# Optimization experiments

Measured on AMD Instinct MI355X. Metric: run time of the kernel, lower is better.

## Reference

```python
import jax, jax.numpy as jnp
import numpy as np

N_BUSES = 2000
W1, W2, W3, LMBDA = 1.0, 1.0, 1.0, 0.1


def setup_inputs() -> dict:
    key = jax.random.key(0)
    k0, k1, k2, k3, k4 = jax.random.split(key, 5)
    B, E = 32, 6000
    x = jax.random.normal(k0, (B * N_BUSES, 6), jnp.float32)
    edge_attr = jax.random.normal(k1, (B * E, 2), jnp.float32)
    edge_index = jax.random.randint(k2, (2, B * E), 0, N_BUSES)
    outputs = jax.random.normal(k3, (B * N_BUSES, 2), jnp.float32)
    labels = jax.random.normal(k4, (B * N_BUSES, 2), jnp.float32)
    return {"x": x, "edge_attr": edge_attr, "edge_index": edge_index,
            "outputs": outputs, "labels": labels}


def _physics_terms(x, edge_attr, edge_index, outputs):
    B = x.shape[0] // N_BUSES
    # Vpred: complex voltage prediction, (B, N, 1)
    Vpred = (outputs[:, 0] + 1j * outputs[:, 1]).astype(jnp.complex64)
    Vpred = Vpred.reshape(B, N_BUSES, 1)
    nf = x.reshape(B, N_BUSES, 6)
    ea = edge_attr.reshape(B, -1, 2)
    E = ea.shape[1]
    ei = edge_index.reshape(2, B, E) % N_BUSES  # (2, B, E)
    S = (nf[:, :, 0] + 1j * nf[:, :, 1]).astype(jnp.complex64)  # (B, N)
    Vm = nf[:, :, 2]
    bus_type = nf[:, :, 3:6]
    adm = (ea[:, :, 0] + 1j * ea[:, :, 1]).astype(jnp.complex64)  # (B, E)
    # scatter edge admittances into dense Y (B, N, N)
    b_idx = jnp.arange(B)[:, None]
    Y = jnp.zeros((B, N_BUSES, N_BUSES), jnp.complex64)
    Y = Y.at[b_idx, ei[0], ei[1]].set(adm)
    # Spred = V * conj(Y @ V)
    YV = jnp.matmul(Y, Vpred)                      # (B, N, 1)
    Spred = (Vpred * jnp.conj(YV))[:, :, 0]        # (B, N)
    S_mean = jnp.mean(S, axis=1, keepdims=True)
    S_inverse = jnp.where(S != 0, 1.0 / S, 1.0 / S_mean)
    S_inverse_norm = jnp.abs(S_inverse)
    result1 = ((Spred - S) ** 2) * bus_type[:, :, 0]                    # complex
    result2 = ((Spred.real - S.real) ** 2) * bus_type[:, :, 1]          # real
    Vm_mean = jnp.mean(Vm, axis=1, keepdims=True)
    Vm_inverse = jnp.where(Vm != 0, 1.0 / Vm, 1.0 / Vm_mean)
    D1 = S_inverse_norm * (result1 + result2)                           # complex
    Vmag = jnp.abs(Vpred[:, :, 0])
    D2 = jnp.abs(Vmag * (bus_type[:, :, 1] + bus_type[:, :, 2]) - Vm) * Vm_inverse
    D3 = jnp.abs(Vpred[:, :, 0].imag * bus_type[:, :, 2]) * Vm_inverse
    return jnp.mean(D1), jnp.mean(D2), jnp.mean(D3)


def reference(x, edge_attr, edge_index, outputs, labels):
    d1, d2, d3 = _physics_terms(x, edge_attr, edge_index, outputs)
    physics_loss = W1 * d1 + W2 * d2 + W3 * d3  # complex (D1 is complex, as in torch)
    mse = jnp.mean((outputs - labels) ** 2)
    loss = mse + LMBDA * physics_loss
    return loss, physics_loss, d1, d2, d3
```

## Files before the change

### kernel.cpp

```cpp
#include <hip/hip_runtime.h>

typedef unsigned long long ull;

#define N_BUSES     2000
#define BATCH       32
#define EDGES_PER_B 6000
#define TOTAL_BUSES (BATCH * N_BUSES)
#define TOTAL_EDGES (BATCH * EDGES_PER_B)

#define SPLIT   16
#define BUS_PER (N_BUSES / SPLIT)
#define TPB     512
#define NBLOCKS (BATCH * SPLIT)

#define HBITS 10
#define HSIZE (1 << HBITS)
#define HMASK (HSIZE - 1)

__device__ __forceinline__ unsigned hash_key(int key) {
    return ((unsigned)key * 2654435761u) >> (32 - HBITS);
}

__global__ __launch_bounds__(TPB)
void fused_split(const float* __restrict__ x, const float* __restrict__ ea,
                 const int* __restrict__ ei, const float* __restrict__ outputs,
                 const float* __restrict__ labels, double* __restrict__ part) {
    __shared__ ull slots[HSIZE];
    __shared__ float yv_sh[2 * BUS_PER];
    __shared__ double red[5][TPB / 64];
    __shared__ float bst[3];

    const int blk = blockIdx.x;
    const int b = blk / SPLIT;
    const int p = blk % SPLIT;
    const int r0 = p * BUS_PER;
    const int tid = threadIdx.x;
    const int wave = tid >> 6, lane = tid & 63;

    for (int k = tid; k < HSIZE; k += TPB) slots[k] = 0ULL;
    for (int k = tid; k < 2 * BUS_PER; k += TPB) yv_sh[k] = 0.0f;

    {
        double sre = 0.0, sim = 0.0, svm = 0.0;
        for (int i = tid; i < N_BUSES; i += TPB) {
            const float* row = x + (size_t)(b * N_BUSES + i) * 6;
            sre += (double)row[0];
            sim += (double)row[1];
            svm += (double)row[2];
        }
        for (int off = 32; off > 0; off >>= 1) {
            sre += __shfl_down(sre, off, 64);
            sim += __shfl_down(sim, off, 64);
            svm += __shfl_down(svm, off, 64);
        }
        if (lane == 0) { red[0][wave] = sre; red[1][wave] = sim; red[2][wave] = svm; }
        __syncthreads();
        if (tid == 0) {
            double a = 0, c = 0, d = 0;
            for (int w = 0; w < TPB / 64; w++) { a += red[0][w]; c += red[1][w]; d += red[2][w]; }
            bst[0] = (float)(a / N_BUSES);
            bst[1] = (float)(c / N_BUSES);
            bst[2] = (float)(d / N_BUSES);
        }
        __syncthreads();
    }

    for (int e = tid; e < EDGES_PER_B; e += TPB) {
        int m = b * EDGES_PER_B + e;
        int i = ei[m] % N_BUSES;
        if (i < r0 || i >= r0 + BUS_PER) continue;
        int j = ei[TOTAL_EDGES + m] % N_BUSES;
        int key = i * N_BUSES + j;
        ull tag = (ull)(unsigned)(key + 1) << 13;
        ull packed = tag | (unsigned)e;
        unsigned h = hash_key(key);
        while (true) {
            ull old = atomicCAS(&slots[h], 0ULL, packed);
            if (old == 0ULL) break;
            if ((old >> 13) == (ull)(unsigned)(key + 1)) { atomicMax(&slots[h], packed); break; }
            h = (h + 1) & HMASK;
        }
    }
    __syncthreads();

    for (int e = tid; e < EDGES_PER_B; e += TPB) {
        int m = b * EDGES_PER_B + e;
        int i = ei[m] % N_BUSES;
        if (i < r0 || i >= r0 + BUS_PER) continue;
        int j = ei[TOTAL_EDGES + m] % N_BUSES;
        int key = i * N_BUSES + j;
        unsigned h = hash_key(key);
        ull s;
        while (((s = slots[h]) >> 13) != (ull)(unsigned)(key + 1)) h = (h + 1) & HMASK;
        if ((int)(s & 0x1FFFULL) != e) continue;
        float2 a = ((const float2*)ea)[m];
        float2 v = ((const float2*)outputs)[b * N_BUSES + j];
        int il = i - r0;
        atomicAdd(&yv_sh[2 * il],     a.x * v.x - a.y * v.y);
        atomicAdd(&yv_sh[2 * il + 1], a.x * v.y + a.y * v.x);
    }
    __syncthreads();

    double t0 = 0.0, t1 = 0.0, t2 = 0.0, t3 = 0.0, t4 = 0.0;
    for (int il = tid; il < BUS_PER; il += TPB) {
        int idx = b * N_BUSES + r0 + il;
        const float2* row2 = (const float2*)(x + (size_t)idx * 6);
        float2 q0 = row2[0], q1 = row2[1], q2 = row2[2];
        float sre = q0.x, sim = q0.y, Vm = q1.x;
        float bt0 = q1.y, bt1 = q2.x, bt2 = q2.y;
        float2 v = ((const float2*)outputs)[idx];
        float yvr = yv_sh[2 * il], yvi = yv_sh[2 * il + 1];
        float spr = v.x * yvr + v.y * yvi;
        float spi = v.y * yvr - v.x * yvi;
        float ir, ii;
        if (sre != 0.0f || sim != 0.0f) {
            float den = sre * sre + sim * sim;
            ir = sre / den; ii = -sim / den;
        } else {
            float mr = bst[0], mi = bst[1];
            float den = mr * mr + mi * mi;
            ir = mr / den; ii = -mi / den;
        }
        float sinv_norm = sqrtf(ir * ir + ii * ii);
        float cr = spr - sre, ci = spi - sim;
        t0 += (double)(sinv_norm * ((cr * cr - ci * ci) * bt0 + (cr * cr) * bt1));
        t1 += (double)(sinv_norm * (2.0f * cr * ci * bt0));
        float vminv = (Vm != 0.0f) ? (1.0f / Vm) : (1.0f / bst[2]);
        float vmag = sqrtf(v.x * v.x + v.y * v.y);
        t2 += (double)(fabsf(vmag * (bt1 + bt2) - Vm) * vminv);
        t3 += (double)(fabsf(v.y * bt2) * vminv);
        float2 l = ((const float2*)labels)[idx];
        float e0 = v.x - l.x, e1 = v.y - l.y;
        t4 += (double)(e0 * e0 + e1 * e1);
    }
    for (int off = 32; off > 0; off >>= 1) {
        t0 += __shfl_down(t0, off, 64);
        t1 += __shfl_down(t1, off, 64);
        t2 += __shfl_down(t2, off, 64);
        t3 += __shfl_down(t3, off, 64);
        t4 += __shfl_down(t4, off, 64);
    }
    __syncthreads();
    if (lane == 0) {
        red[0][wave] = t0; red[1][wave] = t1; red[2][wave] = t2;
        red[3][wave] = t3; red[4][wave] = t4;
    }
    __syncthreads();
    if (tid == 0) {
        double a0 = 0, a1 = 0, a2 = 0, a3 = 0, a4 = 0;
        for (int w = 0; w < TPB / 64; w++) {
            a0 += red[0][w]; a1 += red[1][w]; a2 += red[2][w];
            a3 += red[3][w]; a4 += red[4][w];
        }
        part[blk * 5 + 0] = a0; part[blk * 5 + 1] = a1; part[blk * 5 + 2] = a2;
        part[blk * 5 + 3] = a3; part[blk * 5 + 4] = a4;
    }
}

__global__ __launch_bounds__(TPB)
void finalize(const double* __restrict__ part, float* __restrict__ out, int out_size) {
    int tid = threadIdx.x;
    int wave = tid >> 6, lane = tid & 63;
    double v0 = part[tid * 5 + 0], v1 = part[tid * 5 + 1], v2 = part[tid * 5 + 2];
    double v3 = part[tid * 5 + 3], v4 = part[tid * 5 + 4];
    for (int off = 32; off > 0; off >>= 1) {
        v0 += __shfl_down(v0, off, 64);
        v1 += __shfl_down(v1, off, 64);
        v2 += __shfl_down(v2, off, 64);
        v3 += __shfl_down(v3, off, 64);
        v4 += __shfl_down(v4, off, 64);
    }
    __shared__ double sh[5][TPB / 64];
    if (lane == 0) {
        sh[0][wave] = v0; sh[1][wave] = v1; sh[2][wave] = v2;
        sh[3][wave] = v3; sh[4][wave] = v4;
    }
    __syncthreads();
    if (tid == 0) {
        double a0 = 0, a1 = 0, a2 = 0, a3 = 0, a4 = 0;
        for (int w = 0; w < TPB / 64; w++) {
            a0 += sh[0][w]; a1 += sh[1][w]; a2 += sh[2][w];
            a3 += sh[3][w]; a4 += sh[4][w];
        }
        double inv = 1.0 / (double)TOTAL_BUSES;
        double d1re = a0 * inv, d1im = a1 * inv;
        double d2 = a2 * inv, d3 = a3 * inv;
        double mse = a4 / (2.0 * (double)TOTAL_BUSES);
        double phre = d1re + d2 + d3, phim = d1im;
        double lre = mse + 0.1 * phre, lim = 0.1 * phim;
        if (out_size == 8) {
            out[0] = (float)lre;  out[1] = (float)lim;
            out[2] = (float)phre; out[3] = (float)phim;
            out[4] = (float)d1re; out[5] = (float)d1im;
            out[6] = (float)d2;   out[7] = (float)d3;
        } else {
            float vals[5] = {(float)lre, (float)phre, (float)d1re, (float)d2, (float)d3};
            int n = out_size < 5 ? out_size : 5;
            for (int k = 0; k < n; k++) out[k] = vals[k];
            for (int k = 5; k < out_size && k < 64; k++) out[k] = 0.0f;
        }
    }
}

extern "C" void kernel_launch(void* const* d_in, const int* in_sizes, int n_in,
                              void* d_out, int out_size, void* d_ws, size_t ws_size,
                              hipStream_t stream) {
    const float* x       = (const float*)d_in[0];
    const float* ea      = (const float*)d_in[1];
    const int*   ei      = (const int*)d_in[2];
    const float* outputs = (const float*)d_in[3];
    const float* labels  = (const float*)d_in[4];
    double* part = (double*)d_ws;

    fused_split<<<NBLOCKS, TPB, 0, stream>>>(x, ea, ei, outputs, labels, part);
    finalize<<<1, TPB, 0, stream>>>(part, (float*)d_out, out_size);
}
```

Measured before the change: 97.85 us.

## Single-pass hash dedup with deposed-edge correction, lazy fallback means, 1024-thread blocks

Merges the two hash passes into one: the last-writer-wins winner adds its admittance product and subtracts the product of the edge it displaced, so no second probe pass is needed. Edge indices are preloaded into registers, and blocks now have 1024 threads, one per hash slot and per local bus. The per-batch mean reduction over all 2000 buses now runs only when a bus with zero S or Vm exists, with those buses handled serially by thread 0. The risks are float rounding from the subtract-correction, which can differ slightly from the reference, and a cap of 64 pending buses per block.

```diff
diff --git a/kernel.cpp b/kernel.cpp
--- a/kernel.cpp
+++ b/kernel.cpp
@@ -10,8 +10,9 @@
 
 #define SPLIT   16
 #define BUS_PER (N_BUSES / SPLIT)
-#define TPB     512
+#define TPB     1024
 #define NBLOCKS (BATCH * SPLIT)
+#define EPT     6
 
 #define HBITS 10
 #define HSIZE (1 << HBITS)
@@ -28,7 +29,10 @@
     __shared__ ull slots[HSIZE];
     __shared__ float yv_sh[2 * BUS_PER];
     __shared__ double red[5][TPB / 64];
+    __shared__ double red2[3][TPB / 64];
     __shared__ float bst[3];
+    __shared__ int pend[64];
+    __shared__ int npend;
 
     const int blk = blockIdx.x;
     const int b = blk / SPLIT;
@@ -37,10 +41,114 @@
     const int tid = threadIdx.x;
     const int wave = tid >> 6, lane = tid & 63;
 
-    for (int k = tid; k < HSIZE; k += TPB) slots[k] = 0ULL;
-    for (int k = tid; k < 2 * BUS_PER; k += TPB) yv_sh[k] = 0.0f;
-
-    {
+    int iv[EPT], jv[EPT];
+#pragma unroll
+    for (int k = 0; k < EPT; k++) {
+        int e = tid + k * TPB;
+        if (e < EDGES_PER_B) {
+            iv[k] = ei[b * EDGES_PER_B + e];
+            jv[k] = ei[TOTAL_EDGES + b * EDGES_PER_B + e];
+        } else { iv[k] = -1; jv[k] = 0; }
+    }
+
+    slots[tid] = 0ULL;
+    if (tid < 2 * BUS_PER) yv_sh[tid] = 0.0f;
+    if (tid == 0) npend = 0;
+    __syncthreads();
+
+#pragma unroll
+    for (int k = 0; k < EPT; k++) {
+        int e = tid + k * TPB;
+        if (iv[k] < 0) continue;
+        int i = iv[k] % N_BUSES;
+        if (i < r0 || i >= r0 + BUS_PER) continue;
+        int j = jv[k] % N_BUSES;
+        int key = i * N_BUSES + j;
+        ull tag = (ull)(unsigned)(key + 1) << 13;
+        ull packed = tag | (unsigned)e;
+        unsigned h = hash_key(key);
+        int deposed = -1;
+        bool we_add = false;
+        while (true) {
+            ull old = atomicCAS(&slots[h], 0ULL, packed);
+            if (old == 0ULL) { we_add = true; break; }
+            if ((old >> 13) == (ull)(unsigned)(key + 1)) {
+                ull prev = atomicMax(&slots[h], packed);
+                if (prev < packed) { we_add = true; deposed = (int)(prev & 0x1FFFULL); }
+                break;
+            }
+            h = (h + 1) & HMASK;
+        }
+        if (we_add) {
+            float2 v = ((const float2*)outputs)[b * N_BUSES + j];
+            float2 a = ((const float2*)ea)[b * EDGES_PER_B + e];
+            float addr = a.x * v.x - a.y * v.y;
+            float addi = a.x * v.y + a.y * v.x;
+            if (deposed >= 0) {
+                float2 ap = ((const float2*)ea)[b * EDGES_PER_B + deposed];
+                addr -= ap.x * v.x - ap.y * v.y;
+                addi -= ap.x * v.y + ap.y * v.x;
+            }
+            int il = i - r0;
+            atomicAdd(&yv_sh[2 * il],     addr);
+            atomicAdd(&yv_sh[2 * il + 1], addi);
+        }
+    }
+    __syncthreads();
+
+    double t0 = 0.0, t1 = 0.0, t2 = 0.0, t3 = 0.0, t4 = 0.0;
+    if (tid < BUS_PER) {
+        int il = tid;
+        int idx = b * N_BUSES + r0 + il;
+        const float2* row2 = (const float2*)(x + (size_t)idx * 6);
+        float2 q0 = row2[0], q1 = row2[1], q2 = row2[2];
+        float sre = q0.x, sim = q0.y, Vm = q1.x;
+        float bt0 = q1.y, bt1 = q2.x, bt2 = q2.y;
+        if ((sre == 0.0f && sim == 0.0f) || Vm == 0.0f) {
+            int pp = atomicAdd(&npend, 1);
+            if (pp < 64) pend[pp] = il;
+        } else {
+            float2 v = ((const float2*)outputs)[idx];
+            float yvr = yv_sh[2 * il], yvi = yv_sh[2 * il + 1];
+            float spr = v.x * yvr + v.y * yvi;
+            float spi = v.y * yvr - v.x * yvi;
+            float den = sre * sre + sim * sim;
+            float ir = sre / den, ii = -sim / den;
+            float sinv_norm = sqrtf(ir * ir + ii * ii);
+            float cr = spr - sre, ci = spi - sim;
+            t0 = (double)(sinv_norm * ((cr * cr - ci * ci) * bt0 + (cr * cr) * bt1));
+            t1 = (double)(sinv_norm * (2.0f * cr * ci * bt0));
+            float vminv = 1.0f / Vm;
+            float vmag = sqrtf(v.x * v.x + v.y * v.y);
+            t2 = (double)(fabsf(vmag * (bt1 + bt2) - Vm) * vminv);
+            t3 = (double)(fabsf(v.y * bt2) * vminv);
+            float2 l = ((const float2*)labels)[idx];
+            float e0 = v.x - l.x, e1 = v.y - l.y;
+            t4 = (double)(e0 * e0 + e1 * e1);
+        }
+    }
+    for (int off = 32; off > 0; off >>= 1) {
+        t0 += __shfl_down(t0, off, 64);
+        t1 += __shfl_down(t1, off, 64);
+        t2 += __shfl_down(t2, off, 64);
+        t3 += __shfl_down(t3, off, 64);
+        t4 += __shfl_down(t4, off, 64);
+    }
+    if (lane == 0) {
+        red[0][wave] = t0; red[1][wave] = t1; red[2][wave] = t2;
+        red[3][wave] = t3; red[4][wave] = t4;
+    }
+    __syncthreads();
+
+    double a0 = 0, a1 = 0, a2 = 0, a3 = 0, a4 = 0;
+    if (tid == 0) {
+        for (int w = 0; w < TPB / 64; w++) {
+            a0 += red[0][w]; a1 += red[1][w]; a2 += red[2][w];
+            a3 += red[3][w]; a4 += red[4][w];
+        }
+    }
+
+    if (npend > 0) {
         double sre = 0.0, sim = 0.0, svm = 0.0;
         for (int i = tid; i < N_BUSES; i += TPB) {
             const float* row = x + (size_t)(b * N_BUSES + i) * 6;
@@ -53,111 +161,60 @@
             sim += __shfl_down(sim, off, 64);
             svm += __shfl_down(svm, off, 64);
         }
-        if (lane == 0) { red[0][wave] = sre; red[1][wave] = sim; red[2][wave] = svm; }
+        if (lane == 0) { red2[0][wave] = sre; red2[1][wave] = sim; red2[2][wave] = svm; }
         __syncthreads();
         if (tid == 0) {
-            double a = 0, c = 0, d = 0;
-            for (int w = 0; w < TPB / 64; w++) { a += red[0][w]; c += red[1][w]; d += red[2][w]; }
-            bst[0] = (float)(a / N_BUSES);
-            bst[1] = (float)(c / N_BUSES);
-            bst[2] = (float)(d / N_BUSES);
+            double sa = 0, sb = 0, sc = 0;
+            for (int w = 0; w < TPB / 64; w++) { sa += red2[0][w]; sb += red2[1][w]; sc += red2[2][w]; }
+            bst[0] = (float)(sa / N_BUSES);
+            bst[1] = (float)(sb / N_BUSES);
+            bst[2] = (float)(sc / N_BUSES);
         }
         __syncthreads();
-    }
-
-    for (int e = tid; e < EDGES_PER_B; e += TPB) {
-        int m = b * EDGES_PER_B + e;
-        int i = ei[m] % N_BUSES;
-        if (i < r0 || i >= r0 + BUS_PER) continue;
-        int j = ei[TOTAL_EDGES + m] % N_BUSES;
-        int key = i * N_BUSES + j;
-        ull tag = (ull)(unsigned)(key + 1) << 13;
-        ull packed = tag | (unsigned)e;
-        unsigned h = hash_key(key);
-        while (true) {
-            ull old = atomicCAS(&slots[h], 0ULL, packed);
-            if (old == 0ULL) break;
-            if ((old >> 13) == (ull)(unsigned)(key + 1)) { atomicMax(&slots[h], packed); break; }
-            h = (h + 1) & HMASK;
-        }
-    }
-    __syncthreads();
-
-    for (int e = tid; e < EDGES_PER_B; e += TPB) {
-        int m = b * EDGES_PER_B + e;
-        int i = ei[m] % N_BUSES;
-        if (i < r0 || i >= r0 + BUS_PER) continue;
-        int j = ei[TOTAL_EDGES + m] % N_BUSES;
-        int key = i * N_BUSES + j;
-        unsigned h = hash_key(key);
-        ull s;
-        while (((s = slots[h]) >> 13) != (ull)(unsigned)(key + 1)) h = (h + 1) & HMASK;
-        if ((int)(s & 0x1FFFULL) != e) continue;
-        float2 a = ((const float2*)ea)[m];
-        float2 v = ((const float2*)outputs)[b * N_BUSES + j];
-        int il = i - r0;
-        atomicAdd(&yv_sh[2 * il],     a.x * v.x - a.y * v.y);
-        atomicAdd(&yv_sh[2 * il + 1], a.x * v.y + a.y * v.x);
-    }
-    __syncthreads();
-
-    double t0 = 0.0, t1 = 0.0, t2 = 0.0, t3 = 0.0, t4 = 0.0;
-    for (int il = tid; il < BUS_PER; il += TPB) {
-        int idx = b * N_BUSES + r0 + il;
-        const float2* row2 = (const float2*)(x + (size_t)idx * 6);
-        float2 q0 = row2[0], q1 = row2[1], q2 = row2[2];
-        float sre = q0.x, sim = q0.y, Vm = q1.x;
-        float bt0 = q1.y, bt1 = q2.x, bt2 = q2.y;
-        float2 v = ((const float2*)outputs)[idx];
-        float yvr = yv_sh[2 * il], yvi = yv_sh[2 * il + 1];
-        float spr = v.x * yvr + v.y * yvi;
-        float spi = v.y * yvr - v.x * yvi;
-        float ir, ii;
-        if (sre != 0.0f || sim != 0.0f) {
-            float den = sre * sre + sim * sim;
-            ir = sre / den; ii = -sim / den;
-        } else {
-            float mr = bst[0], mi = bst[1];
-            float den = mr * mr + mi * mi;
-            ir = mr / den; ii = -mi / den;
-        }
-        float sinv_norm = sqrtf(ir * ir + ii * ii);
-        float cr = spr - sre, ci = spi - sim;
-        t0 += (double)(sinv_norm * ((cr * cr - ci * ci) * bt0 + (cr * cr) * bt1));
-        t1 += (double)(sinv_norm * (2.0f * cr * ci * bt0));
-        float vminv = (Vm != 0.0f) ? (1.0f / Vm) : (1.0f / bst[2]);
-        float vmag = sqrtf(v.x * v.x + v.y * v.y);
-        t2 += (double)(fabsf(vmag * (bt1 + bt2) - Vm) * vminv);
-        t3 += (double)(fabsf(v.y * bt2) * vminv);
-        float2 l = ((const float2*)labels)[idx];
-        float e0 = v.x - l.x, e1 = v.y - l.y;
-        t4 += (double)(e0 * e0 + e1 * e1);
-    }
-    for (int off = 32; off > 0; off >>= 1) {
-        t0 += __shfl_down(t0, off, 64);
-        t1 += __shfl_down(t1, off, 64);
-        t2 += __shfl_down(t2, off, 64);
-        t3 += __shfl_down(t3, off, 64);
-        t4 += __shfl_down(t4, off, 64);
-    }
-    __syncthreads();
-    if (lane == 0) {
-        red[0][wave] = t0; red[1][wave] = t1; red[2][wave] = t2;
-        red[3][wave] = t3; red[4][wave] = t4;
-    }
-    __syncthreads();
+        if (tid == 0) {
+            int np = npend < 64 ? npend : 64;
+            for (int q = 0; q < np; q++) {
+                int il = pend[q];
+                int idx = b * N_BUSES + r0 + il;
+                const float2* row2 = (const float2*)(x + (size_t)idx * 6);
+                float2 q0 = row2[0], q1 = row2[1], q2 = row2[2];
+                float sr = q0.x, si = q0.y, Vm = q1.x;
+                float bt0 = q1.y, bt1 = q2.x, bt2 = q2.y;
+                float2 v = ((const float2*)outputs)[idx];
+                float yvr = yv_sh[2 * il], yvi = yv_sh[2 * il + 1];
+                float spr = v.x * yvr + v.y * yvi;
+                float spi = v.y * yvr - v.x * yvi;
+                float ir, ii;
+                if (sr != 0.0f || si != 0.0f) {
+                    float den = sr * sr + si * si;
+                    ir = sr / den; ii = -si / den;
+                } else {
+                    float mr = bst[0], mi = bst[1];
+                    float den = mr * mr + mi * mi;
+                    ir = mr / den; ii = -mi / den;
+                }
+                float sinv_norm = sqrtf(ir * ir + ii * ii);
+                float cr = spr - sr, ci = spi - si;
+                a0 += (double)(sinv_norm * ((cr * cr - ci * ci) * bt0 + (cr * cr) * bt1));
+                a1 += (double)(sinv_norm * (2.0f * cr * ci * bt0));
+                float vminv = (Vm != 0.0f) ? (1.0f / Vm) : (1.0f / bst[2]);
+                float vmag = sqrtf(v.x * v.x + v.y * v.y);
+                a2 += (double)(fabsf(vmag * (bt1 + bt2) - Vm) * vminv);
+                a3 += (double)(fabsf(v.y * bt2) * vminv);
+                float2 l = ((const float2*)labels)[idx];
+                float e0 = v.x - l.x, e1 = v.y - l.y;
+                a4 += (double)(e0 * e0 + e1 * e1);
+            }
+        }
+    }
+
     if (tid == 0) {
-        double a0 = 0, a1 = 0, a2 = 0, a3 = 0, a4 = 0;
-        for (int w = 0; w < TPB / 64; w++) {
-            a0 += red[0][w]; a1 += red[1][w]; a2 += red[2][w];
-            a3 += red[3][w]; a4 += red[4][w];
-        }
         part[blk * 5 + 0] = a0; part[blk * 5 + 1] = a1; part[blk * 5 + 2] = a2;
         part[blk * 5 + 3] = a3; part[blk * 5 + 4] = a4;
     }
 }
 
-__global__ __launch_bounds__(TPB)
+__global__ __launch_bounds__(512)
 void finalize(const double* __restrict__ part, float* __restrict__ out, int out_size) {
     int tid = threadIdx.x;
     int wave = tid >> 6, lane = tid & 63;
@@ -170,7 +227,7 @@
         v3 += __shfl_down(v3, off, 64);
         v4 += __shfl_down(v4, off, 64);
     }
-    __shared__ double sh[5][TPB / 64];
+    __shared__ double sh[5][8];
     if (lane == 0) {
         sh[0][wave] = v0; sh[1][wave] = v1; sh[2][wave] = v2;
         sh[3][wave] = v3; sh[4][wave] = v4;
@@ -178,7 +235,7 @@
     __syncthreads();
     if (tid == 0) {
         double a0 = 0, a1 = 0, a2 = 0, a3 = 0, a4 = 0;
-        for (int w = 0; w < TPB / 64; w++) {
+        for (int w = 0; w < 8; w++) {
             a0 += sh[0][w]; a1 += sh[1][w]; a2 += sh[2][w];
             a3 += sh[3][w]; a4 += sh[4][w];
         }
@@ -213,5 +270,5 @@
     double* part = (double*)d_ws;
 
     fused_split<<<NBLOCKS, TPB, 0, stream>>>(x, ea, ei, outputs, labels, part);
-    finalize<<<1, TPB, 0, stream>>>(part, (float*)d_out, out_size);
-}
+    finalize<<<1, 512, 0, stream>>>(part, (float*)d_out, out_size);
+}
```

Measured after the change: 84.30 us. 1.16x faster.
